# Optimization experiments

Hardware: AMD Instinct MI355X
Metric: run time of the kernel (lower is better)

## Reference

```python
import jax, jax.numpy as jnp
import numpy as np

DIM = 512; H = 8; TEMP_LEN = 16; TARGET_LEN = 22
NT = TEMP_LEN ** 2          # 256 temp tokens
NS = TARGET_LEN ** 2        # 484 target tokens
N = NT + NS                 # 740
HD = DIM // H
SCALE = HD ** -0.5
EPS = 1e-5
B = 16


def _bias_index(L):
    coords = np.stack(np.meshgrid(np.arange(L), np.arange(L), indexing='ij')).reshape(2, -1)
    rel = (coords[:, :, None] - coords[:, None, :]).transpose(1, 2, 0)  # [L^2, L^2, 2]
    rel[..., 0] += L - 1
    rel[..., 1] += L - 1
    rel[..., 0] *= 2 * L - 1
    return jnp.asarray(rel.sum(-1))  # [L^2, L^2] indices into (2L-1)^2 table

TEMP_IDX = _bias_index(TEMP_LEN)
TARGET_IDX = _bias_index(TARGET_LEN)


def setup_inputs() -> dict:
    key = jax.random.key(0)
    ctr = iter(range(100))
    def nrm(shape, s=1.0):
        return jax.random.normal(jax.random.fold_in(key, next(ctr)), shape, jnp.float32) * s
    def uni(shape):
        return jax.random.uniform(jax.random.fold_in(key, next(ctr)), shape, jnp.float32, 0.5, 1.5)
    d = {'x': nrm((B, N, DIM))}
    for nm in ('q', 'k', 'v'):
        d[f'conv_{nm}_w'] = nrm((DIM, 1, 3, 3), 0.2)   # depthwise 3x3, groups=DIM
        d[f'bn_{nm}_g'] = 1.0 + nrm((DIM,), 0.1)
        d[f'bn_{nm}_b'] = nrm((DIM,), 0.1)
        d[f'bn_{nm}_m'] = nrm((DIM,), 0.1)
        d[f'bn_{nm}_v'] = uni((DIM,))
    for nm in ('q', 'k', 'v', 'p'):
        d[f'w{nm}'] = nrm((DIM, DIM), DIM ** -0.5)
        d[f'b{nm}'] = nrm((DIM,), 0.01)
    d['rpb_target'] = nrm(((2 * TARGET_LEN - 1) ** 2, H), 0.0002)
    d['rpb_temp'] = nrm(((2 * TEMP_LEN - 1) ** 2, 1), 0.0002)
    d['tt_bias'] = nrm((H, 1, NT), 0.0002)       # temp_target_bias_table
    d['tg_tm_bias'] = nrm((H, NS, 1), 0.0002)    # target_temp_bias_table
    return d


def _dwconv_bn(z, w, g, b, m, v):
    # z: [B, C, Hh, Ww]; depthwise conv + BatchNorm2d (inference stats)
    y = jax.lax.conv_general_dilated(z, w, (1, 1), ((1, 1), (1, 1)),
                                     dimension_numbers=('NCHW', 'OIHW', 'NCHW'),
                                     feature_group_count=DIM)
    inv = (g * jax.lax.rsqrt(v + EPS))[None, :, None, None]
    return (y - m[None, :, None, None]) * inv + b[None, :, None, None]


def reference(x, conv_q_w, bn_q_g, bn_q_b, bn_q_m, bn_q_v,
              conv_k_w, bn_k_g, bn_k_b, bn_k_m, bn_k_v,
              conv_v_w, bn_v_g, bn_v_b, bn_v_m, bn_v_v,
              wq, bq, wk, bk, wv, bv, wp, bp,
              rpb_target, rpb_temp, tt_bias, tg_tm_bias):
    Bb = x.shape[0]
    to_img = lambda t, L: t.transpose(0, 2, 1).reshape(Bb, DIM, L, L)
    to_seq = lambda t: t.reshape(Bb, DIM, -1).transpose(0, 2, 1)
    ti = to_img(x[:, :NT], TEMP_LEN)
    tg = to_img(x[:, NT:], TARGET_LEN)

    def conv_branch(w, g, b, m, v):
        return jnp.concatenate([to_seq(_dwconv_bn(ti, w, g, b, m, v)),
                                to_seq(_dwconv_bn(tg, w, g, b, m, v))], axis=1)

    q = conv_branch(conv_q_w, bn_q_g, bn_q_b, bn_q_m, bn_q_v) @ wq + bq
    k = conv_branch(conv_k_w, bn_k_g, bn_k_b, bn_k_m, bn_k_v) @ wk + bk
    v = conv_branch(conv_v_w, bn_v_g, bn_v_b, bn_v_m, bn_v_v) @ wv + bv

    heads = lambda t: t.reshape(Bb, -1, H, HD).transpose(0, 2, 1, 3)
    qtm, ktm, vtm = heads(q[:, :NT]), heads(k[:, :NT]), heads(v[:, :NT])
    qta, kh, vh = heads(q[:, NT:]), heads(k), heads(v)

    # gathered relative-position bias tables
    target_bias = rpb_target[TARGET_IDX.reshape(-1)].reshape(NS, NS, H).transpose(2, 0, 1)  # [H,NS,NS]
    temp_bias = rpb_temp[TEMP_IDX.reshape(-1)].reshape(NT, NT, 1).transpose(2, 0, 1)        # [1,NT,NT]
    padding = tt_bias + tg_tm_bias                                                          # [H,NS,NT]
    rel = jnp.concatenate([padding, target_bias], axis=2)                                   # [H,NS,N]

    # target -> all attention
    attn = jax.nn.softmax(jnp.einsum('bhqd,bhkd->bhqk', qta, kh) * SCALE + rel, axis=-1)
    out_t = jnp.einsum('bhqk,bhkd->bhqd', attn, vh).transpose(0, 2, 1, 3).reshape(Bb, NS, DIM)

    # temp -> temp attention (bias broadcast over heads)
    attn2 = jax.nn.softmax(jnp.einsum('bhqd,bhkd->bhqk', qtm, ktm) * SCALE + temp_bias, axis=-1)
    out_m = jnp.einsum('bhqk,bhkd->bhqd', attn2, vtm).transpose(0, 2, 1, 3).reshape(Bb, NT, DIM)

    return jnp.concatenate([out_m, out_t], axis=1) @ wp + bp
```

## Files before the change

### kernel.cpp

```cpp
#include <hip/hip_runtime.h>
#include <hip/hip_bf16.h>

typedef unsigned short u16;
typedef unsigned int u32;
typedef __attribute__((ext_vector_type(8))) short short8;
typedef __attribute__((ext_vector_type(4))) float f32x4;

#define NTOK 740
#define NTMP 256
#define NTGT 484
#define DM   512
#define MH   8
#define MROWS 11840
#define KPAD 768

__device__ __forceinline__ float b2f(u16 u) {
    union { unsigned int i; float f; } x; x.i = ((unsigned int)u) << 16; return x.f;
}
__device__ __forceinline__ u16 f2b(float f) {
    union { float f; unsigned int i; } x; x.f = f;
    unsigned int r = x.i + 0x7FFFu + ((x.i >> 16) & 1u);
    return (u16)(r >> 16);
}
struct alignas(8) us4 { u16 x, y, z, w; };

__device__ __forceinline__ void gload16(const void* g, void* l) {
    __builtin_amdgcn_global_load_lds(
        (const __attribute__((address_space(1))) void*)g,
        (__attribute__((address_space(3))) void*)l, 16, 0, 0);
}

__global__ __launch_bounds__(256) void transpose512(const float* __restrict__ W,
                                                    u16* __restrict__ WT) {
    __shared__ float t[32][33];
    int bx = blockIdx.x, by = blockIdx.y;
    int tx = threadIdx.x;
    for (int i = threadIdx.y; i < 32; i += 8)
        t[i][tx] = W[(size_t)(by * 32 + i) * 512 + bx * 32 + tx];
    __syncthreads();
    for (int i = threadIdx.y; i < 32; i += 8)
        WT[(size_t)(bx * 32 + i) * 512 + by * 32 + tx] = f2b(t[tx][i]);
}

__global__ __launch_bounds__(512) void prep_conv(const float* __restrict__ cw,
                                                 const float* __restrict__ g,
                                                 const float* __restrict__ bb,
                                                 const float* __restrict__ m,
                                                 const float* __restrict__ v,
                                                 float* __restrict__ cwf,
                                                 float* __restrict__ shift) {
    const int tap = blockIdx.x, c = threadIdx.x;
    const float inv = g[c] * rsqrtf(v[c] + 1e-5f);
    cwf[tap * DM + c] = cw[c * 9 + tap] * inv;
    if (tap == 0) shift[c] = bb[c] - m[c] * inv;
}

__global__ __launch_bounds__(256) void conv_bn3(
    const float* __restrict__ x,
    const float* __restrict__ cwf0, const float* __restrict__ sh0,
    const float* __restrict__ cwf1, const float* __restrict__ sh1,
    const float* __restrict__ cwf2, const float* __restrict__ sh2,
    u16* __restrict__ o0, u16* __restrict__ o1, u16* __restrict__ o2) {
    const int bn = blockIdx.x * 2 + (threadIdx.x >> 7);
    const int c = (threadIdx.x & 127) * 4;
    const int b = bn / NTOK, n = bn % NTOK;
    const bool tmp = n < NTMP;
    const int L = tmp ? 16 : 22, base = tmp ? 0 : NTMP, p = n - base;
    const int ph = p / L, pw = p % L;
    float4 xv[9];
#pragma unroll
    for (int tap = 0; tap < 9; ++tap) {
        const int dh = tap / 3 - 1, dw = tap % 3 - 1;
        const int h2 = ph + dh, w2 = pw + dw;
        const bool ok = (h2 >= 0 && h2 < L && w2 >= 0 && w2 < L);
        xv[tap] = ok ? *(const float4*)(x + (size_t)(b * NTOK + base + h2 * L + w2) * DM + c)
                     : float4{0.f, 0.f, 0.f, 0.f};
    }
    const size_t o = (size_t)bn * DM + c;
    const float* cwf[3] = {cwf0, cwf1, cwf2};
    const float* sh[3]  = {sh0, sh1, sh2};
    u16* out[3] = {o0, o1, o2};
#pragma unroll
    for (int br = 0; br < 3; ++br) {
        float4 acc = *(const float4*)(sh[br] + c);
#pragma unroll
        for (int tap = 0; tap < 9; ++tap) {
            const float4 wv = *(const float4*)(cwf[br] + tap * DM + c);
            acc.x = fmaf(wv.x, xv[tap].x, acc.x);
            acc.y = fmaf(wv.y, xv[tap].y, acc.y);
            acc.z = fmaf(wv.z, xv[tap].z, acc.z);
            acc.w = fmaf(wv.w, xv[tap].w, acc.w);
        }
        us4 r;
        r.x = f2b(acc.x); r.y = f2b(acc.y); r.z = f2b(acc.z); r.w = f2b(acc.w);
        *(us4*)(out[br] + o) = r;
    }
}

template <int MODE>
__global__ __launch_bounds__(256) void gemm64(const u16* __restrict__ A,
                                              const u16* __restrict__ BT,
                                              const float* __restrict__ bias,
                                              void* __restrict__ Cout) {
    __shared__ u16 As[2][64 * 32];
    __shared__ u16 Bs[2][128 * 32];
    const int tid = threadIdx.x;
    const int gm0 = blockIdx.x * 64;
    const int gn0 = blockIdx.y * 128;
    const int lane = tid & 63, w = tid >> 6;
    const int lr = lane & 15, lg = lane >> 4;
    const int wm = (w >> 1) * 32, wn = (w & 1) * 64;

    const int srow4 = lane >> 2;
    const int sc = (lane & 3) ^ (srow4 & 3);
    const u16* asrc  = A  + (size_t)(gm0 + w * 16 + srow4) * 512 + sc * 8;
    const u16* bsrc0 = BT + (size_t)(gn0 + w * 32 + srow4) * 512 + sc * 8;
    const u16* bsrc1 = BT + (size_t)(gn0 + w * 32 + 16 + srow4) * 512 + sc * 8;

#define STAGEG(bf, koff) do { \
    gload16(asrc + (koff),  &As[bf][w * 512]); \
    gload16(bsrc0 + (koff), &Bs[bf][w * 1024]); \
    gload16(bsrc1 + (koff), &Bs[bf][w * 1024 + 512]); \
} while (0)

    f32x4 acc[2][4] = {};
    STAGEG(0, 0);
    for (int kt = 0; kt < 16; ++kt) {
        const int cur = kt & 1;
        if (kt < 15) {
            STAGEG(cur ^ 1, (kt + 1) * 32);
            asm volatile("s_waitcnt vmcnt(3)" ::: "memory");
        } else {
            asm volatile("s_waitcnt vmcnt(0)" ::: "memory");
        }
        __syncthreads();
        short8 af[2], bfr[4];
#pragma unroll
        for (int i = 0; i < 2; ++i)
            af[i] = *(const short8*)&As[cur][(wm + i * 16 + lr) * 32 + (lg ^ (lr & 3)) * 8];
#pragma unroll
        for (int j = 0; j < 4; ++j)
            bfr[j] = *(const short8*)&Bs[cur][(wn + j * 16 + lr) * 32 + (lg ^ (lr & 3)) * 8];
#pragma unroll
        for (int i = 0; i < 2; ++i)
#pragma unroll
            for (int j = 0; j < 4; ++j)
                acc[i][j] = __builtin_amdgcn_mfma_f32_16x16x32_bf16(af[i], bfr[j], acc[i][j], 0, 0, 0);
        __syncthreads();
    }
#undef STAGEG

#pragma unroll
    for (int i = 0; i < 2; ++i)
#pragma unroll
        for (int j = 0; j < 4; ++j) {
            const int gc = gn0 + wn + j * 16 + lr;
            const float bv = bias[gc];
#pragma unroll
            for (int r = 0; r < 4; ++r) {
                const int gr = gm0 + wm + i * 16 + lg * 4 + r;
                const float val = acc[i][j][r] + bv;
                if constexpr (MODE == 0) {
                    ((u16*)Cout)[(size_t)gr * 512 + gc] = f2b(val);
                } else if constexpr (MODE == 1) {
                    ((float*)Cout)[(size_t)gr * 512 + gc] = val;
                } else {
                    const int b2 = gr / NTOK, k = gr - b2 * NTOK;
                    const int hh = gc >> 6, d = gc & 63;
                    ((u16*)Cout)[((size_t)(b2 * MH + hh) * 64 + d) * KPAD + k] = f2b(val);
                }
            }
        }
}

__global__ __launch_bounds__(256) void build_bias_t(const float* __restrict__ rpb_t,
                                                    const float* __restrict__ tt,
                                                    const float* __restrict__ tg,
                                                    u16* __restrict__ btab) {
    const int q = blockIdx.x, h = blockIdx.y;
    const int qh = q / 22, qw = q % 22;
    const float tgv = tg[h * NTGT + q];
    for (int k = threadIdx.x; k < KPAD; k += 256) {
        float val;
        if (k < NTMP) val = tt[h * NTMP + k] + tgv;
        else if (k < NTOK) {
            const int kj = k - NTMP, kh = kj / 22, kw = kj % 22;
            val = rpb_t[((qh - kh + 21) * 43 + (qw - kw + 21)) * MH + h];
        } else val = -1e30f;
        btab[((size_t)(h * NTGT + q)) * KPAD + k] = f2b(val);
    }
}
__global__ __launch_bounds__(256) void build_bias_m(const float* __restrict__ rpb_m,
                                                    u16* __restrict__ mtab) {
    const int q = blockIdx.x, k = threadIdx.x;
    const int qh = q >> 4, qw = q & 15, kh = k >> 4, kw = k & 15;
    mtab[q * 256 + k] = f2b(rpb_m[(qh - kh + 15) * 31 + (qw - kw + 15)]);
}

__global__ __launch_bounds__(256) void attn_all(const u16* __restrict__ qb,
                                                const u16* __restrict__ kb,
                                                const u16* __restrict__ vbT,
                                                const u16* __restrict__ btab,
                                                const u16* __restrict__ mtab,
                                                u16* __restrict__ attb) {
    __shared__ u16 Ks[2][32][64];
    __shared__ u16 VTs[2][64][32];
    __shared__ u16 Pb[4][16][32];

    const int bx = blockIdx.x, h = blockIdx.y, b = blockIdx.z;
    const bool tgt = bx < 8;
    const int q0 = (tgt ? bx : bx - 8) * 64;
    const int NKr = tgt ? NTOK : NTMP;
    const int NCH = tgt ? 24 : 8;
    const int QTOT = tgt ? NTGT : NTMP;
    const int QOFF = tgt ? NTMP : 0;
    const int tid = threadIdx.x;
    const int w = tid >> 6, lane = tid & 63;
    const int lq = lane & 15, lg = lane >> 4;
    const size_t brow = (size_t)b * NTOK;

    int qmine = q0 + w * 16 + lq;
    if (qmine > QTOT - 1) qmine = QTOT - 1;
    const u16* trow = tgt ? (btab + ((size_t)(h * NTGT + qmine)) * KPAD)
                          : (mtab + qmine * 256);

    short8 qf[2];
#pragma unroll
    for (int dc = 0; dc < 2; ++dc)
        qf[dc] = *(const short8*)(qb + (brow + QOFF + qmine) * DM + h * 64 + dc * 32 + lg * 8);

    const int krow = tid >> 3, ksc = tid & 7;
    const int vrow = tid >> 2, vsc = tid & 3;
    const u16* kptr = kb + brow * DM + h * 64 + ksc * 8;
    const u16* vptr = vbT + (size_t)(b * MH + h) * 64 * KPAD + (size_t)vrow * KPAD + vsc * 8;

    float mrun = -1e30f, lrun = 0.f;
    f32x4 oT[4] = {};

    {
        int4 kv = (krow < NKr) ? *(const int4*)(kptr + (size_t)krow * DM) : int4{0, 0, 0, 0};
        *(int4*)&Ks[0][krow][(ksc ^ (krow & 7)) * 8] = kv;
        int4 vv = *(const int4*)(vptr);
        *(int4*)&VTs[0][vrow][(vsc ^ (vrow & 3)) * 8] = vv;
    }
    us4 bc0 = *(const us4*)(trow + lg * 4);
    us4 bc1 = *(const us4*)(trow + 16 + lg * 4);
    __syncthreads();

    for (int kc = 0; kc < NCH; ++kc) {
        const int cur = kc & 1, nxt = cur ^ 1;
        const bool more = (kc + 1 < NCH);
        int4 nk = {0, 0, 0, 0}, nv = {0, 0, 0, 0};
        us4 bn0 = {0, 0, 0, 0}, bn1 = {0, 0, 0, 0};
        if (more) {
            const int key = (kc + 1) * 32 + krow;
            if (key < NKr) nk = *(const int4*)(kptr + (size_t)key * DM);
            nv = *(const int4*)(vptr + (kc + 1) * 32);
            bn0 = *(const us4*)(trow + (kc + 1) * 32 + lg * 4);
            bn1 = *(const us4*)(trow + (kc + 1) * 32 + 16 + lg * 4);
        }

        f32x4 s0 = {}, s1 = {};
#pragma unroll
        for (int dc = 0; dc < 2; ++dc) {
            short8 a0 = *(const short8*)&Ks[cur][lq][((dc * 4 + lg) ^ (lq & 7)) * 8];
            short8 a1 = *(const short8*)&Ks[cur][16 + lq][((dc * 4 + lg) ^ (lq & 7)) * 8];
            s0 = __builtin_amdgcn_mfma_f32_16x16x32_bf16(a0, qf[dc], s0, 0, 0, 0);
            s1 = __builtin_amdgcn_mfma_f32_16x16x32_bf16(a1, qf[dc], s1, 0, 0, 0);
        }
        float sv[8];
        sv[0] = fmaf(s0[0], 0.125f, b2f(bc0.x)); sv[1] = fmaf(s0[1], 0.125f, b2f(bc0.y));
        sv[2] = fmaf(s0[2], 0.125f, b2f(bc0.z)); sv[3] = fmaf(s0[3], 0.125f, b2f(bc0.w));
        sv[4] = fmaf(s1[0], 0.125f, b2f(bc1.x)); sv[5] = fmaf(s1[1], 0.125f, b2f(bc1.y));
        sv[6] = fmaf(s1[2], 0.125f, b2f(bc1.z)); sv[7] = fmaf(s1[3], 0.125f, b2f(bc1.w));

        float cm = sv[0];
#pragma unroll
        for (int i = 1; i < 8; ++i) cm = fmaxf(cm, sv[i]);
        cm = fmaxf(cm, __shfl_xor(cm, 16));
        cm = fmaxf(cm, __shfl_xor(cm, 32));
        const float mnew = fmaxf(mrun, cm);
        const float alpha = __expf(mrun - mnew);
        float pv[8]; float psum = 0.f;
#pragma unroll
        for (int i = 0; i < 8; ++i) { pv[i] = __expf(sv[i] - mnew); psum += pv[i]; }
        psum += __shfl_xor(psum, 16);
        psum += __shfl_xor(psum, 32);
        lrun = lrun * alpha + psum;
        mrun = mnew;

        us4 pw0, pw1;
        pw0.x = f2b(pv[0]); pw0.y = f2b(pv[1]); pw0.z = f2b(pv[2]); pw0.w = f2b(pv[3]);
        pw1.x = f2b(pv[4]); pw1.y = f2b(pv[5]); pw1.z = f2b(pv[6]); pw1.w = f2b(pv[7]);
        *(us4*)&Pb[w][lq][(((lg >> 1)) ^ (lq & 3)) * 8 + (lg & 1) * 4] = pw0;
        *(us4*)&Pb[w][lq][((2 + (lg >> 1)) ^ (lq & 3)) * 8 + (lg & 1) * 4] = pw1;

#pragma unroll
        for (int t = 0; t < 4; ++t)
#pragma unroll
            for (int r = 0; r < 4; ++r) oT[t][r] *= alpha;

        asm volatile("s_waitcnt lgkmcnt(0)" ::: "memory");

        short8 pf = *(const short8*)&Pb[w][lq][(lg ^ (lq & 3)) * 8];
#pragma unroll
        for (int t = 0; t < 4; ++t) {
            short8 vf = *(const short8*)&VTs[cur][t * 16 + lq][(lg ^ (lq & 3)) * 8];
            oT[t] = __builtin_amdgcn_mfma_f32_16x16x32_bf16(vf, pf, oT[t], 0, 0, 0);
        }

        if (more) {
            *(int4*)&Ks[nxt][krow][(ksc ^ (krow & 7)) * 8] = nk;
            *(int4*)&VTs[nxt][vrow][(vsc ^ (vrow & 3)) * 8] = nv;
            bc0 = bn0; bc1 = bn1;
        }
        __syncthreads();
    }

    const float linv = 1.f / lrun;
    const int qrow = q0 + w * 16 + lq;
    if (qrow < QTOT) {
        u16* op = attb + (brow + QOFF + qrow) * DM + h * 64;
#pragma unroll
        for (int t = 0; t < 4; ++t) {
            us4 o;
            o.x = f2b(oT[t][0] * linv); o.y = f2b(oT[t][1] * linv);
            o.z = f2b(oT[t][2] * linv); o.w = f2b(oT[t][3] * linv);
            *(us4*)(op + t * 16 + lg * 4) = o;
        }
    }
}

extern "C" void kernel_launch(void* const* d_in, const int* in_sizes, int n_in,
                              void* d_out, int out_size, void* d_ws, size_t ws_size,
                              hipStream_t stream) {
    const float* x = (const float*)d_in[0];
    const float* convw[3] = {(const float*)d_in[1], (const float*)d_in[6], (const float*)d_in[11]};
    const float* bng[3]   = {(const float*)d_in[2], (const float*)d_in[7], (const float*)d_in[12]};
    const float* bnb[3]   = {(const float*)d_in[3], (const float*)d_in[8], (const float*)d_in[13]};
    const float* bnm[3]   = {(const float*)d_in[4], (const float*)d_in[9], (const float*)d_in[14]};
    const float* bnv[3]   = {(const float*)d_in[5], (const float*)d_in[10], (const float*)d_in[15]};
    const float* w[4]     = {(const float*)d_in[16], (const float*)d_in[18], (const float*)d_in[20], (const float*)d_in[22]};
    const float* bias[4]  = {(const float*)d_in[17], (const float*)d_in[19], (const float*)d_in[21], (const float*)d_in[23]};
    const float* rpb_t = (const float*)d_in[24];
    const float* rpb_m = (const float*)d_in[25];
    const float* tt    = (const float*)d_in[26];
    const float* tg    = (const float*)d_in[27];

    char* ws = (char*)d_ws;
    u16* wT[4];
    for (int i = 0; i < 4; ++i) wT[i] = (u16*)(ws + (size_t)i * 524288);
    const size_t SEQ = (size_t)MROWS * DM * 2;
    u16* cbq  = (u16*)(ws + 2097152);
    u16* cbk  = (u16*)(ws + 2097152 + SEQ);
    u16* cbv  = (u16*)(ws + 2097152 + 2 * SEQ);
    u16* kbuf = (u16*)(ws + 2097152 + 3 * SEQ);
    u16* vbT  = (u16*)(ws + 2097152 + 4 * SEQ);
    u16* btab = (u16*)(ws + 2097152 + 4 * SEQ + 12582912);
    u16* mtab = (u16*)(ws + 2097152 + 4 * SEQ + 12582912 + 5947392);
    float* cwf = (float*)(ws + 2097152 + 4 * SEQ + 12582912 + 5947392 + 131072);
    float* shf = cwf + 3 * 9 * DM;
    u16* qbuf = cbv;
    u16* attb = cbq;

    for (int i = 0; i < 4; ++i)
        transpose512<<<dim3(16, 16), dim3(32, 8), 0, stream>>>(w[i], wT[i]);
    build_bias_t<<<dim3(NTGT, MH), 256, 0, stream>>>(rpb_t, tt, tg, btab);
    build_bias_m<<<256, 256, 0, stream>>>(rpb_m, mtab);
    for (int br = 0; br < 3; ++br)
        prep_conv<<<9, 512, 0, stream>>>(convw[br], bng[br], bnb[br], bnm[br], bnv[br],
                                         cwf + br * 9 * DM, shf + br * DM);

    conv_bn3<<<MROWS / 2, 256, 0, stream>>>(x,
        cwf, shf, cwf + 9 * DM, shf + DM, cwf + 18 * DM, shf + 2 * DM,
        cbq, cbk, cbv);

    gemm64<2><<<dim3(185, 4), 256, 0, stream>>>(cbv, wT[2], bias[2], vbT);
    gemm64<0><<<dim3(185, 4), 256, 0, stream>>>(cbq, wT[0], bias[0], qbuf);
    gemm64<0><<<dim3(185, 4), 256, 0, stream>>>(cbk, wT[1], bias[1], kbuf);

    attn_all<<<dim3(12, 8, 16), 256, 0, stream>>>(qbuf, kbuf, vbT, btab, mtab, attb);

    gemm64<1><<<dim3(185, 4), 256, 0, stream>>>(attb, wT[3], bias[3], d_out);
}
```

Baseline: 199.5 us.

## Merge setup/QKV launches and streamline attention softmax with exp2 and lazy rescale

Batches the four weight transposes, three conv prep kernels, and the Q and K projection GEMMs into fewer launches using a z-grid dimension. In attention, it folds log2(e) into the bias tables and scale so it can use the native exp2, and skips output rescaling when no row maximum grows. It also packs bf16 conversions, raises wave priority around MFMA blocks, and changes the LDS swizzle for V and P. These target launch overhead and softmax ALU cost, at the cost of more complex indexing and a slight precision change from bf16 rounding of pre-scaled biases.

Measured after the change: 186.3 us. 6.6% less time.

```diff
diff --git a/kernel.cpp b/kernel.cpp
--- a/kernel.cpp
+++ b/kernel.cpp
@@ -13,6 +13,7 @@
 #define MH   8
 #define MROWS 11840
 #define KPAD 768
+#define LOG2E 1.4426950408889634f
 
 __device__ __forceinline__ float b2f(u16 u) {
     union { unsigned int i; float f; } x; x.i = ((unsigned int)u) << 16; return x.f;
@@ -22,6 +23,14 @@
     unsigned int r = x.i + 0x7FFFu + ((x.i >> 16) & 1u);
     return (u16)(r >> 16);
 }
+__device__ __forceinline__ u32 pk2(float a, float b) {
+    union { __hip_bfloat162 h; u32 u; } p;
+    p.h = __float22bfloat162_rn(float2{a, b});
+    return p.u;
+}
+__device__ __forceinline__ float fexp2(float x) {
+    return __builtin_amdgcn_exp2f(x);
+}
 struct alignas(8) us4 { u16 x, y, z, w; };
 
 __device__ __forceinline__ void gload16(const void* g, void* l) {
@@ -30,9 +39,15 @@
         (__attribute__((address_space(3))) void*)l, 16, 0, 0);
 }
 
-__global__ __launch_bounds__(256) void transpose512(const float* __restrict__ W,
-                                                    u16* __restrict__ WT) {
+__global__ __launch_bounds__(256) void transpose4(const float* __restrict__ w0,
+                                                  const float* __restrict__ w1,
+                                                  const float* __restrict__ w2,
+                                                  const float* __restrict__ w3,
+                                                  u16* __restrict__ wTbase) {
     __shared__ float t[32][33];
+    const int z = blockIdx.z;
+    const float* W = z == 0 ? w0 : z == 1 ? w1 : z == 2 ? w2 : w3;
+    u16* WT = wTbase + (size_t)z * 262144;
     int bx = blockIdx.x, by = blockIdx.y;
     int tx = threadIdx.x;
     for (int i = threadIdx.y; i < 32; i += 8)
@@ -42,24 +57,28 @@
         WT[(size_t)(bx * 32 + i) * 512 + by * 32 + tx] = f2b(t[tx][i]);
 }
 
-__global__ __launch_bounds__(512) void prep_conv(const float* __restrict__ cw,
-                                                 const float* __restrict__ g,
-                                                 const float* __restrict__ bb,
-                                                 const float* __restrict__ m,
-                                                 const float* __restrict__ v,
-                                                 float* __restrict__ cwf,
-                                                 float* __restrict__ shift) {
-    const int tap = blockIdx.x, c = threadIdx.x;
+__global__ __launch_bounds__(512) void prep_conv3(
+    const float* __restrict__ cw0, const float* __restrict__ g0, const float* __restrict__ bb0,
+    const float* __restrict__ m0, const float* __restrict__ v0,
+    const float* __restrict__ cw1, const float* __restrict__ g1, const float* __restrict__ bb1,
+    const float* __restrict__ m1, const float* __restrict__ v1,
+    const float* __restrict__ cw2, const float* __restrict__ g2, const float* __restrict__ bb2,
+    const float* __restrict__ m2, const float* __restrict__ v2,
+    float* __restrict__ cwfb, float* __restrict__ shb) {
+    const int tap = blockIdx.x, br = blockIdx.y, c = threadIdx.x;
+    const float* cw = br == 0 ? cw0 : br == 1 ? cw1 : cw2;
+    const float* g  = br == 0 ? g0  : br == 1 ? g1  : g2;
+    const float* bb = br == 0 ? bb0 : br == 1 ? bb1 : bb2;
+    const float* m  = br == 0 ? m0  : br == 1 ? m1  : m2;
+    const float* v  = br == 0 ? v0  : br == 1 ? v1  : v2;
     const float inv = g[c] * rsqrtf(v[c] + 1e-5f);
-    cwf[tap * DM + c] = cw[c * 9 + tap] * inv;
-    if (tap == 0) shift[c] = bb[c] - m[c] * inv;
+    cwfb[(br * 9 + tap) * DM + c] = cw[c * 9 + tap] * inv;
+    if (tap == 0) shb[br * DM + c] = bb[c] - m[c] * inv;
 }
 
 __global__ __launch_bounds__(256) void conv_bn3(
     const float* __restrict__ x,
-    const float* __restrict__ cwf0, const float* __restrict__ sh0,
-    const float* __restrict__ cwf1, const float* __restrict__ sh1,
-    const float* __restrict__ cwf2, const float* __restrict__ sh2,
+    const float* __restrict__ cwfb, const float* __restrict__ shb,
     u16* __restrict__ o0, u16* __restrict__ o1, u16* __restrict__ o2) {
     const int bn = blockIdx.x * 2 + (threadIdx.x >> 7);
     const int c = (threadIdx.x & 127) * 4;
@@ -77,15 +96,13 @@
                      : float4{0.f, 0.f, 0.f, 0.f};
     }
     const size_t o = (size_t)bn * DM + c;
-    const float* cwf[3] = {cwf0, cwf1, cwf2};
-    const float* sh[3]  = {sh0, sh1, sh2};
     u16* out[3] = {o0, o1, o2};
 #pragma unroll
     for (int br = 0; br < 3; ++br) {
-        float4 acc = *(const float4*)(sh[br] + c);
+        float4 acc = *(const float4*)(shb + br * DM + c);
 #pragma unroll
         for (int tap = 0; tap < 9; ++tap) {
-            const float4 wv = *(const float4*)(cwf[br] + tap * DM + c);
+            const float4 wv = *(const float4*)(cwfb + (br * 9 + tap) * DM + c);
             acc.x = fmaf(wv.x, xv[tap].x, acc.x);
             acc.y = fmaf(wv.y, xv[tap].y, acc.y);
             acc.z = fmaf(wv.z, xv[tap].z, acc.z);
@@ -97,78 +114,99 @@
     }
 }
 
-template <int MODE>
-__global__ __launch_bounds__(256) void gemm64(const u16* __restrict__ A,
-                                              const u16* __restrict__ BT,
-                                              const float* __restrict__ bias,
-                                              void* __restrict__ Cout) {
+#define GEMM_BODY(A, BT)                                                             \
+    const int tid = threadIdx.x;                                                     \
+    const int gm0 = blockIdx.x * 64;                                                 \
+    const int gn0 = blockIdx.y * 128;                                                \
+    const int lane = tid & 63, w = tid >> 6;                                         \
+    const int lr = lane & 15, lg = lane >> 4;                                        \
+    const int wm = (w >> 1) * 32, wn = (w & 1) * 64;                                 \
+    const int srow4 = lane >> 2;                                                     \
+    const int sc = (lane & 3) ^ (srow4 & 3);                                         \
+    const u16* asrc  = A  + (size_t)(gm0 + w * 16 + srow4) * 512 + sc * 8;           \
+    const u16* bsrc0 = BT + (size_t)(gn0 + w * 32 + srow4) * 512 + sc * 8;           \
+    const u16* bsrc1 = BT + (size_t)(gn0 + w * 32 + 16 + srow4) * 512 + sc * 8;      \
+    f32x4 acc[2][4] = {};                                                            \
+    gload16(asrc, &As[0][w * 512]);                                                  \
+    gload16(bsrc0, &Bs[0][w * 1024]);                                                \
+    gload16(bsrc1, &Bs[0][w * 1024 + 512]);                                          \
+    for (int kt = 0; kt < 16; ++kt) {                                                \
+        const int cur = kt & 1;                                                      \
+        if (kt < 15) {                                                               \
+            gload16(asrc + (kt + 1) * 32, &As[cur ^ 1][w * 512]);                    \
+            gload16(bsrc0 + (kt + 1) * 32, &Bs[cur ^ 1][w * 1024]);                  \
+            gload16(bsrc1 + (kt + 1) * 32, &Bs[cur ^ 1][w * 1024 + 512]);            \
+            asm volatile("s_waitcnt vmcnt(3)" ::: "memory");                         \
+        } else {                                                                     \
+            asm volatile("s_waitcnt vmcnt(0)" ::: "memory");                         \
+        }                                                                            \
+        __syncthreads();                                                             \
+        short8 af[2], bfr[4];                                                        \
+        _Pragma("unroll")                                                            \
+        for (int i = 0; i < 2; ++i)                                                  \
+            af[i] = *(const short8*)&As[cur][(wm + i * 16 + lr) * 32 + (lg ^ (lr & 3)) * 8]; \
+        _Pragma("unroll")                                                            \
+        for (int j = 0; j < 4; ++j)                                                  \
+            bfr[j] = *(const short8*)&Bs[cur][(wn + j * 16 + lr) * 32 + (lg ^ (lr & 3)) * 8]; \
+        _Pragma("unroll")                                                            \
+        for (int i = 0; i < 2; ++i)                                                  \
+            _Pragma("unroll")                                                        \
+            for (int j = 0; j < 4; ++j)                                              \
+                acc[i][j] = __builtin_amdgcn_mfma_f32_16x16x32_bf16(af[i], bfr[j], acc[i][j], 0, 0, 0); \
+        __syncthreads();                                                             \
+    }
+
+__global__ __launch_bounds__(256) void gemm_qkv(
+    const u16* __restrict__ Aq, const u16* __restrict__ Ak, const u16* __restrict__ Av,
+    const u16* __restrict__ wTb, const float* __restrict__ bq,
+    const float* __restrict__ bk, const float* __restrict__ bv,
+    u16* __restrict__ qout, u16* __restrict__ kout, u16* __restrict__ vbT, int zbase) {
     __shared__ u16 As[2][64 * 32];
     __shared__ u16 Bs[2][128 * 32];
-    const int tid = threadIdx.x;
-    const int gm0 = blockIdx.x * 64;
-    const int gn0 = blockIdx.y * 128;
-    const int lane = tid & 63, w = tid >> 6;
-    const int lr = lane & 15, lg = lane >> 4;
-    const int wm = (w >> 1) * 32, wn = (w & 1) * 64;
-
-    const int srow4 = lane >> 2;
-    const int sc = (lane & 3) ^ (srow4 & 3);
-    const u16* asrc  = A  + (size_t)(gm0 + w * 16 + srow4) * 512 + sc * 8;
-    const u16* bsrc0 = BT + (size_t)(gn0 + w * 32 + srow4) * 512 + sc * 8;
-    const u16* bsrc1 = BT + (size_t)(gn0 + w * 32 + 16 + srow4) * 512 + sc * 8;
-
-#define STAGEG(bf, koff) do { \
-    gload16(asrc + (koff),  &As[bf][w * 512]); \
-    gload16(bsrc0 + (koff), &Bs[bf][w * 1024]); \
-    gload16(bsrc1 + (koff), &Bs[bf][w * 1024 + 512]); \
-} while (0)
-
-    f32x4 acc[2][4] = {};
-    STAGEG(0, 0);
-    for (int kt = 0; kt < 16; ++kt) {
-        const int cur = kt & 1;
-        if (kt < 15) {
-            STAGEG(cur ^ 1, (kt + 1) * 32);
-            asm volatile("s_waitcnt vmcnt(3)" ::: "memory");
-        } else {
-            asm volatile("s_waitcnt vmcnt(0)" ::: "memory");
-        }
-        __syncthreads();
-        short8 af[2], bfr[4];
-#pragma unroll
-        for (int i = 0; i < 2; ++i)
-            af[i] = *(const short8*)&As[cur][(wm + i * 16 + lr) * 32 + (lg ^ (lr & 3)) * 8];
-#pragma unroll
-        for (int j = 0; j < 4; ++j)
-            bfr[j] = *(const short8*)&Bs[cur][(wn + j * 16 + lr) * 32 + (lg ^ (lr & 3)) * 8];
-#pragma unroll
-        for (int i = 0; i < 2; ++i)
-#pragma unroll
-            for (int j = 0; j < 4; ++j)
-                acc[i][j] = __builtin_amdgcn_mfma_f32_16x16x32_bf16(af[i], bfr[j], acc[i][j], 0, 0, 0);
-        __syncthreads();
-    }
-#undef STAGEG
-
+    const int z = blockIdx.z + zbase;
+    const u16* A = z == 0 ? Aq : z == 1 ? Ak : Av;
+    const u16* BT = wTb + (size_t)z * 262144;
+    const float* bias = z == 0 ? bq : z == 1 ? bk : bv;
+    GEMM_BODY(A, BT)
+    u16* lin = z == 0 ? qout : kout;
 #pragma unroll
     for (int i = 0; i < 2; ++i)
 #pragma unroll
         for (int j = 0; j < 4; ++j) {
             const int gc = gn0 + wn + j * 16 + lr;
-            const float bv = bias[gc];
+            const float bvl = bias[gc];
 #pragma unroll
             for (int r = 0; r < 4; ++r) {
                 const int gr = gm0 + wm + i * 16 + lg * 4 + r;
-                const float val = acc[i][j][r] + bv;
-                if constexpr (MODE == 0) {
-                    ((u16*)Cout)[(size_t)gr * 512 + gc] = f2b(val);
-                } else if constexpr (MODE == 1) {
-                    ((float*)Cout)[(size_t)gr * 512 + gc] = val;
-                } else {
+                const float val = acc[i][j][r] + bvl;
+                if (z == 2) {
                     const int b2 = gr / NTOK, k = gr - b2 * NTOK;
                     const int hh = gc >> 6, d = gc & 63;
-                    ((u16*)Cout)[((size_t)(b2 * MH + hh) * 64 + d) * KPAD + k] = f2b(val);
+                    vbT[((size_t)(b2 * MH + hh) * 64 + d) * KPAD + k] = f2b(val);
+                } else {
+                    lin[(size_t)gr * 512 + gc] = f2b(val);
                 }
+            }
+        }
+}
+
+__global__ __launch_bounds__(256) void gemm_out(const u16* __restrict__ Ain,
+                                                const u16* __restrict__ BTin,
+                                                const float* __restrict__ bias,
+                                                float* __restrict__ C) {
+    __shared__ u16 As[2][64 * 32];
+    __shared__ u16 Bs[2][128 * 32];
+    GEMM_BODY(Ain, BTin)
+#pragma unroll
+    for (int i = 0; i < 2; ++i)
+#pragma unroll
+        for (int j = 0; j < 4; ++j) {
+            const int gc = gn0 + wn + j * 16 + lr;
+            const float bvl = bias[gc];
+#pragma unroll
+            for (int r = 0; r < 4; ++r) {
+                const int gr = gm0 + wm + i * 16 + lg * 4 + r;
+                C[(size_t)gr * 512 + gc] = acc[i][j][r] + bvl;
             }
         }
 }
@@ -182,10 +220,10 @@
     const float tgv = tg[h * NTGT + q];
     for (int k = threadIdx.x; k < KPAD; k += 256) {
         float val;
-        if (k < NTMP) val = tt[h * NTMP + k] + tgv;
+        if (k < NTMP) val = (tt[h * NTMP + k] + tgv) * LOG2E;
         else if (k < NTOK) {
             const int kj = k - NTMP, kh = kj / 22, kw = kj % 22;
-            val = rpb_t[((qh - kh + 21) * 43 + (qw - kw + 21)) * MH + h];
+            val = rpb_t[((qh - kh + 21) * 43 + (qw - kw + 21)) * MH + h] * LOG2E;
         } else val = -1e30f;
         btab[((size_t)(h * NTGT + q)) * KPAD + k] = f2b(val);
     }
@@ -194,7 +232,7 @@
                                                     u16* __restrict__ mtab) {
     const int q = blockIdx.x, k = threadIdx.x;
     const int qh = q >> 4, qw = q & 15, kh = k >> 4, kw = k & 15;
-    mtab[q * 256 + k] = f2b(rpb_m[(qh - kh + 15) * 31 + (qw - kw + 15)]);
+    mtab[q * 256 + k] = f2b(rpb_m[(qh - kh + 15) * 31 + (qw - kw + 15)] * LOG2E);
 }
 
 __global__ __launch_bounds__(256) void attn_all(const u16* __restrict__ qb,
@@ -217,7 +255,9 @@
     const int tid = threadIdx.x;
     const int w = tid >> 6, lane = tid & 63;
     const int lq = lane & 15, lg = lane >> 4;
+    const int fq = (lq & 3) ^ ((lq >> 2) & 3);
     const size_t brow = (size_t)b * NTOK;
+    const float SCL = 0.125f * LOG2E;
 
     int qmine = q0 + w * 16 + lq;
     if (qmine > QTOT - 1) qmine = QTOT - 1;
@@ -231,6 +271,7 @@
 
     const int krow = tid >> 3, ksc = tid & 7;
     const int vrow = tid >> 2, vsc = tid & 3;
+    const int fv = (vrow & 3) ^ ((vrow >> 2) & 3);
     const u16* kptr = kb + brow * DM + h * 64 + ksc * 8;
     const u16* vptr = vbT + (size_t)(b * MH + h) * 64 * KPAD + (size_t)vrow * KPAD + vsc * 8;
 
@@ -241,7 +282,7 @@
         int4 kv = (krow < NKr) ? *(const int4*)(kptr + (size_t)krow * DM) : int4{0, 0, 0, 0};
         *(int4*)&Ks[0][krow][(ksc ^ (krow & 7)) * 8] = kv;
         int4 vv = *(const int4*)(vptr);
-        *(int4*)&VTs[0][vrow][(vsc ^ (vrow & 3)) * 8] = vv;
+        *(int4*)&VTs[0][vrow][(vsc ^ fv) * 8] = vv;
     }
     us4 bc0 = *(const us4*)(trow + lg * 4);
     us4 bc1 = *(const us4*)(trow + 16 + lg * 4);
@@ -261,6 +302,7 @@
         }
 
         f32x4 s0 = {}, s1 = {};
+        __builtin_amdgcn_s_setprio(1);
 #pragma unroll
         for (int dc = 0; dc < 2; ++dc) {
             short8 a0 = *(const short8*)&Ks[cur][lq][((dc * 4 + lg) ^ (lq & 7)) * 8];
@@ -268,50 +310,55 @@
             s0 = __builtin_amdgcn_mfma_f32_16x16x32_bf16(a0, qf[dc], s0, 0, 0, 0);
             s1 = __builtin_amdgcn_mfma_f32_16x16x32_bf16(a1, qf[dc], s1, 0, 0, 0);
         }
+        __builtin_amdgcn_s_setprio(0);
         float sv[8];
-        sv[0] = fmaf(s0[0], 0.125f, b2f(bc0.x)); sv[1] = fmaf(s0[1], 0.125f, b2f(bc0.y));
-        sv[2] = fmaf(s0[2], 0.125f, b2f(bc0.z)); sv[3] = fmaf(s0[3], 0.125f, b2f(bc0.w));
-        sv[4] = fmaf(s1[0], 0.125f, b2f(bc1.x)); sv[5] = fmaf(s1[1], 0.125f, b2f(bc1.y));
-        sv[6] = fmaf(s1[2], 0.125f, b2f(bc1.z)); sv[7] = fmaf(s1[3], 0.125f, b2f(bc1.w));
+        sv[0] = fmaf(s0[0], SCL, b2f(bc0.x)); sv[1] = fmaf(s0[1], SCL, b2f(bc0.y));
+        sv[2] = fmaf(s0[2], SCL, b2f(bc0.z)); sv[3] = fmaf(s0[3], SCL, b2f(bc0.w));
+        sv[4] = fmaf(s1[0], SCL, b2f(bc1.x)); sv[5] = fmaf(s1[1], SCL, b2f(bc1.y));
+        sv[6] = fmaf(s1[2], SCL, b2f(bc1.z)); sv[7] = fmaf(s1[3], SCL, b2f(bc1.w));
 
         float cm = sv[0];
 #pragma unroll
         for (int i = 1; i < 8; ++i) cm = fmaxf(cm, sv[i]);
         cm = fmaxf(cm, __shfl_xor(cm, 16));
         cm = fmaxf(cm, __shfl_xor(cm, 32));
-        const float mnew = fmaxf(mrun, cm);
-        const float alpha = __expf(mrun - mnew);
+        if (!__all(cm <= mrun)) {
+            const float mnew = fmaxf(mrun, cm);
+            const float alpha = fexp2(mrun - mnew);
+#pragma unroll
+            for (int t = 0; t < 4; ++t)
+#pragma unroll
+                for (int r = 0; r < 4; ++r) oT[t][r] *= alpha;
+            lrun *= alpha;
+            mrun = mnew;
+        }
         float pv[8]; float psum = 0.f;
 #pragma unroll
-        for (int i = 0; i < 8; ++i) { pv[i] = __expf(sv[i] - mnew); psum += pv[i]; }
+        for (int i = 0; i < 8; ++i) { pv[i] = fexp2(sv[i] - mrun); psum += pv[i]; }
+
+        const int c0 = (((lg >> 1) ^ fq) & 3) * 8 + (lg & 1) * 4;
+        const int c1 = (((2 + (lg >> 1)) ^ fq) & 3) * 8 + (lg & 1) * 4;
+        *(uint2*)&Pb[w][lq][c0] = uint2{pk2(pv[0], pv[1]), pk2(pv[2], pv[3])};
+        *(uint2*)&Pb[w][lq][c1] = uint2{pk2(pv[4], pv[5]), pk2(pv[6], pv[7])};
+
         psum += __shfl_xor(psum, 16);
         psum += __shfl_xor(psum, 32);
-        lrun = lrun * alpha + psum;
-        mrun = mnew;
-
-        us4 pw0, pw1;
-        pw0.x = f2b(pv[0]); pw0.y = f2b(pv[1]); pw0.z = f2b(pv[2]); pw0.w = f2b(pv[3]);
-        pw1.x = f2b(pv[4]); pw1.y = f2b(pv[5]); pw1.z = f2b(pv[6]); pw1.w = f2b(pv[7]);
-        *(us4*)&Pb[w][lq][(((lg >> 1)) ^ (lq & 3)) * 8 + (lg & 1) * 4] = pw0;
-        *(us4*)&Pb[w][lq][((2 + (lg >> 1)) ^ (lq & 3)) * 8 + (lg & 1) * 4] = pw1;
-
-#pragma unroll
-        for (int t = 0; t < 4; ++t)
-#pragma unroll
-            for (int r = 0; r < 4; ++r) oT[t][r] *= alpha;
+        lrun += psum;
 
         asm volatile("s_waitcnt lgkmcnt(0)" ::: "memory");
 
-        short8 pf = *(const short8*)&Pb[w][lq][(lg ^ (lq & 3)) * 8];
+        short8 pf = *(const short8*)&Pb[w][lq][((lg ^ fq) & 3) * 8];
+        __builtin_amdgcn_s_setprio(1);
 #pragma unroll
         for (int t = 0; t < 4; ++t) {
-            short8 vf = *(const short8*)&VTs[cur][t * 16 + lq][(lg ^ (lq & 3)) * 8];
+            short8 vf = *(const short8*)&VTs[cur][t * 16 + lq][((lg ^ fq) & 3) * 8];
             oT[t] = __builtin_amdgcn_mfma_f32_16x16x32_bf16(vf, pf, oT[t], 0, 0, 0);
         }
+        __builtin_amdgcn_s_setprio(0);
 
         if (more) {
             *(int4*)&Ks[nxt][krow][(ksc ^ (krow & 7)) * 8] = nk;
-            *(int4*)&VTs[nxt][vrow][(vsc ^ (vrow & 3)) * 8] = nv;
+            *(int4*)&VTs[nxt][vrow][(vsc ^ fv) * 8] = nv;
             bc0 = bn0; bc1 = bn1;
         }
         __syncthreads();
@@ -322,12 +369,10 @@
     if (qrow < QTOT) {
         u16* op = attb + (brow + QOFF + qrow) * DM + h * 64;
 #pragma unroll
-        for (int t = 0; t < 4; ++t) {
-            us4 o;
-            o.x = f2b(oT[t][0] * linv); o.y = f2b(oT[t][1] * linv);
-            o.z = f2b(oT[t][2] * linv); o.w = f2b(oT[t][3] * linv);
-            *(us4*)(op + t * 16 + lg * 4) = o;
-        }
+        for (int t = 0; t < 4; ++t)
+            *(uint2*)(op + t * 16 + lg * 4) =
+                uint2{pk2(oT[t][0] * linv, oT[t][1] * linv),
+                      pk2(oT[t][2] * linv, oT[t][3] * linv)};
     }
 }
 
@@ -348,8 +393,7 @@
     const float* tg    = (const float*)d_in[27];
 
     char* ws = (char*)d_ws;
-    u16* wT[4];
-    for (int i = 0; i < 4; ++i) wT[i] = (u16*)(ws + (size_t)i * 524288);
+    u16* wTb = (u16*)ws;
     const size_t SEQ = (size_t)MROWS * DM * 2;
     u16* cbq  = (u16*)(ws + 2097152);
     u16* cbk  = (u16*)(ws + 2097152 + SEQ);
@@ -363,23 +407,24 @@
     u16* qbuf = cbv;
     u16* attb = cbq;
 
-    for (int i = 0; i < 4; ++i)
-        transpose512<<<dim3(16, 16), dim3(32, 8), 0, stream>>>(w[i], wT[i]);
+    transpose4<<<dim3(16, 16, 4), dim3(32, 8), 0, stream>>>(w[0], w[1], w[2], w[3], wTb);
+    prep_conv3<<<dim3(9, 3), 512, 0, stream>>>(
+        convw[0], bng[0], bnb[0], bnm[0], bnv[0],
+        convw[1], bng[1], bnb[1], bnm[1], bnv[1],
+        convw[2], bng[2], bnb[2], bnm[2], bnv[2], cwf, shf);
     build_bias_t<<<dim3(NTGT, MH), 256, 0, stream>>>(rpb_t, tt, tg, btab);
     build_bias_m<<<256, 256, 0, stream>>>(rpb_m, mtab);
-    for (int br = 0; br < 3; ++br)
-        prep_conv<<<9, 512, 0, stream>>>(convw[br], bng[br], bnb[br], bnm[br], bnv[br],
-                                         cwf + br * 9 * DM, shf + br * DM);
-
-    conv_bn3<<<MROWS / 2, 256, 0, stream>>>(x,
-        cwf, shf, cwf + 9 * DM, shf + DM, cwf + 18 * DM, shf + 2 * DM,
-        cbq, cbk, cbv);
-
-    gemm64<2><<<dim3(185, 4), 256, 0, stream>>>(cbv, wT[2], bias[2], vbT);
-    gemm64<0><<<dim3(185, 4), 256, 0, stream>>>(cbq, wT[0], bias[0], qbuf);
-    gemm64<0><<<dim3(185, 4), 256, 0, stream>>>(cbk, wT[1], bias[1], kbuf);
+
+    conv_bn3<<<MROWS / 2, 256, 0, stream>>>(x, cwf, shf, cbq, cbk, cbv);
+
+    gemm_qkv<<<dim3(185, 4, 1), 256, 0, stream>>>(cbq, cbk, cbv, wTb,
+                                                  bias[0], bias[1], bias[2],
+                                                  qbuf, kbuf, vbT, 2);
+    gemm_qkv<<<dim3(185, 4, 2), 256, 0, stream>>>(cbq, cbk, cbv, wTb,
+                                                  bias[0], bias[1], bias[2],
+                                                  qbuf, kbuf, vbT, 0);
 
     attn_all<<<dim3(12, 8, 16), 256, 0, stream>>>(qbuf, kbuf, vbT, btab, mtab, attb);
 
-    gemm64<1><<<dim3(185, 4), 256, 0, stream>>>(attb, wT[3], bias[3], d_out);
-}
+    gemm_out<<<dim3(185, 4), 256, 0, stream>>>(attb, wTb + 3 * 262144, bias[3], (float*)d_out);
+}
```
